# Kernel tuning notes

Hardware: AMD Instinct MI355X
Metric: run time of the kernel (lower is better)

Reference implementation:

```python
import jax, jax.numpy as jnp
import numpy as np

N_NODES = 50000
N_EDGES = 800000
N_GRAPHS = 256
IN_DIM = 128
HID = 128
BN_EPS = 1e-5


def setup_inputs() -> dict:
    key = jax.random.key(0)
    ks = jax.random.split(key, 12)
    s = 1.0 / np.sqrt(HID)
    feats = jax.random.normal(ks[0], (N_NODES, IN_DIM), jnp.float32)
    src = jax.random.randint(ks[1], (2, N_EDGES), 0, N_NODES)
    dst = jax.random.randint(ks[2], (2, N_EDGES), 0, N_NODES)
    graph_ids = jnp.sort(jax.random.randint(ks[3], (N_NODES,), 0, N_GRAPHS))
    eps = jnp.full((2, 2), 0.1, jnp.float32)
    Wa = jax.random.normal(ks[4], (2, 2, IN_DIM, HID), jnp.float32) * s
    ba = jnp.zeros((2, 2, HID), jnp.float32)
    bng = jnp.ones((2, 2, HID), jnp.float32)
    bnb = jnp.zeros((2, 2, HID), jnp.float32)
    Wb = jax.random.normal(ks[5], (2, 2, HID, HID), jnp.float32) * s
    bb = jnp.zeros((2, 2, HID), jnp.float32)
    oW1 = jax.random.normal(ks[6], (2 * HID, HID), jnp.float32) * (1.0 / np.sqrt(2 * HID))
    ob1 = jnp.zeros((HID,), jnp.float32)
    oW2 = jax.random.normal(ks[7], (HID, HID), jnp.float32) * s
    ob2 = jnp.zeros((HID,), jnp.float32)
    oW3 = jax.random.normal(ks[8], (HID, 1), jnp.float32) * s
    ob3 = jnp.zeros((1,), jnp.float32)
    return {"feats": feats, "src": src, "dst": dst, "graph_ids": graph_ids,
            "n_graphs": N_GRAPHS, "eps": eps, "Wa": Wa, "ba": ba, "bng": bng,
            "bnb": bnb, "Wb": Wb, "bb": bb, "oW1": oW1, "ob1": ob1,
            "oW2": oW2, "ob2": ob2, "oW3": oW3, "ob3": ob3}


def _gin_layer(h, s, d, eps_l, Wa_l, ba_l, g_l, be_l, Wb_l, bb_l, relu_out):
    # sum-aggregate messages from src to dst over edge list
    N = h.shape[0]
    agg = jax.ops.segment_sum(h[s], d, num_segments=N)  # [N, D]
    x = (1.0 + eps_l) * h + agg
    # MLP_Layer: Linear -> BatchNorm(training stats) -> ReLU -> Linear
    x = x @ Wa_l + ba_l
    mu = jnp.mean(x, axis=0)
    var = jnp.var(x, axis=0)
    x = (x - mu) * jax.lax.rsqrt(var + BN_EPS) * g_l + be_l
    x = jax.nn.relu(x)
    x = x @ Wb_l + bb_l
    return jax.nn.relu(x) if relu_out else x  # GINConv activation (gin1 only)


def reference(feats, src, dst, graph_ids, n_graphs, eps, Wa, ba, bng, bnb,
              Wb, bb, oW1, ob1, oW2, ob2, oW3, ob3):
    outs = []
    for e in range(2):  # one BTGINs encoder per bottom edge type
        h = feats
        for l in range(2):  # gin1 (ReLU) then gin2 (no activation)
            h = _gin_layer(h, src[e], dst[e], eps[e, l], Wa[e, l], ba[e, l],
                           bng[e, l], bnb[e, l], Wb[e, l], bb[e, l], relu_out=(l == 0))
        outs.append(h)
    h = jnp.concatenate(outs, axis=-1)  # [N, 2*HID]
    # readout_nodes op='sum': per-graph segment sum
    hg = jax.ops.segment_sum(h, graph_ids, num_segments=n_graphs)  # [G, 2*HID]
    # out_layers: 3-layer MLP, no BN
    x = jax.nn.relu(hg @ oW1 + ob1)
    x = jax.nn.relu(x @ oW2 + ob2)
    return x @ oW3 + ob3  # [G, 1]
```

## Files before the change

### kernel.cpp

```cpp
#include <hip/hip_runtime.h>

#define NT 50000
#define NE 800000
#define NG 256
#define DIM 128
#define GEMM_B ((NT + 127) / 128)

#define NB 128
#define BW 391
#define PB 196
#define PCH 4096
#define HCN (NB * PB)

typedef short s16x8 __attribute__((ext_vector_type(8)));
typedef float f32x16 __attribute__((ext_vector_type(16)));

__device__ __forceinline__ unsigned short f32_to_bf16(float f) {
    unsigned int u = __float_as_uint(f);
    u += 0x7FFFu + ((u >> 16) & 1u);
    return (unsigned short)(u >> 16);
}
__device__ __forceinline__ float bf16_to_f32(unsigned short h) {
    return __uint_as_float(((unsigned int)h) << 16);
}

__global__ __launch_bounds__(256) void ranges_kernel(const int* __restrict__ gid,
                                                     int* __restrict__ goff) {
    int g = threadIdx.x;
    int lo = 0, hi = NT;
    while (lo < hi) {
        int mid = (lo + hi) >> 1;
        if (gid[mid] < g) lo = mid + 1; else hi = mid;
    }
    goff[g] = lo;
    if (g == 0) goff[NG] = NT;
}

__global__ __launch_bounds__(256) void tobf16_kernel(const float* __restrict__ in,
                                                     unsigned short* __restrict__ out) {
    int i = blockIdx.x * 256 + threadIdx.x;
    if (i >= NT * 32) return;
    float4 v = ((const float4*)in)[i];
    ushort4 o;
    o.x = f32_to_bf16(v.x); o.y = f32_to_bf16(v.y);
    o.z = f32_to_bf16(v.z); o.w = f32_to_bf16(v.w);
    ((ushort4*)out)[i] = o;
}

__global__ __launch_bounds__(256) void csr_part_hist_kernel(
        const int* __restrict__ dstAll, int* __restrict__ hcoarseAll) {
    const int* dst = dstAll + (size_t)blockIdx.y * NE;
    int* hcoarse = hcoarseAll + (size_t)blockIdx.y * HCN;
    __shared__ int h[NB];
    if (threadIdx.x < NB) h[threadIdx.x] = 0;
    __syncthreads();
#pragma unroll
    for (int i = 0; i < PCH / 256; ++i) {
        int e = blockIdx.x * PCH + i * 256 + threadIdx.x;
        if (e < NE) atomicAdd(&h[dst[e] / BW], 1);
    }
    __syncthreads();
    if (threadIdx.x < NB)
        hcoarse[threadIdx.x * PB + blockIdx.x] = h[threadIdx.x];
}

__global__ __launch_bounds__(1024) void csr_scan_kernel(
        const int* __restrict__ hcoarseAll, int* __restrict__ offAll,
        int* __restrict__ bucketBaseAll, int* __restrict__ indptrAll) {
    const int* hcoarse = hcoarseAll + (size_t)blockIdx.x * HCN;
    int* off = offAll + (size_t)blockIdx.x * HCN;
    int* bucketBase = bucketBaseAll + (size_t)blockIdx.x * (NB + 1);
    int* indptr = indptrAll + (size_t)blockIdx.x * (NT + 1);
    __shared__ int ps[1024];
    int t = threadIdx.x;
    const int CH = (HCN + 1023) / 1024;
    int beg = t * CH, end = beg + CH; if (end > HCN) end = HCN;
    int s = 0;
    for (int i = beg; i < end; ++i) s += hcoarse[i];
    ps[t] = s;
    __syncthreads();
    for (int o = 1; o < 1024; o <<= 1) {
        int v = (t >= o) ? ps[t - o] : 0;
        __syncthreads();
        ps[t] += v;
        __syncthreads();
    }
    int run = (t == 0) ? 0 : ps[t - 1];
    for (int i = beg; i < end; ++i) {
        off[i] = run;
        if (i % PB == 0) bucketBase[i / PB] = run;
        run += hcoarse[i];
    }
    if (t == 1023) bucketBase[NB] = NE;
    if (t == 0) indptr[NT] = NE;
}

__global__ __launch_bounds__(256) void csr_scatter_kernel(
        const int* __restrict__ srcAll, const int* __restrict__ dstAll,
        const int* __restrict__ offAll, unsigned int* __restrict__ partAll) {
    const int* src = srcAll + (size_t)blockIdx.y * NE;
    const int* dst = dstAll + (size_t)blockIdx.y * NE;
    const int* off = offAll + (size_t)blockIdx.y * HCN;
    unsigned int* part = partAll + (size_t)blockIdx.y * NE;
    __shared__ int cur[NB];
    if (threadIdx.x < NB) cur[threadIdx.x] = off[threadIdx.x * PB + blockIdx.x];
    __syncthreads();
#pragma unroll
    for (int i = 0; i < PCH / 256; ++i) {
        int e = blockIdx.x * PCH + i * 256 + threadIdx.x;
        if (e < NE) {
            int d = dst[e];
            int b = d / BW;
            int pos = atomicAdd(&cur[b], 1);
            part[pos] = ((unsigned int)(d - b * BW) << 16) | (unsigned int)src[e];
        }
    }
}

__global__ __launch_bounds__(256) void csr_finalize_kernel(
        const unsigned int* __restrict__ partAll,
        const int* __restrict__ bucketBaseAll,
        int* __restrict__ indptrAll, int* __restrict__ esrcAll) {
    const unsigned int* part = partAll + (size_t)blockIdx.y * NE;
    const int* bucketBase = bucketBaseAll + (size_t)blockIdx.y * (NB + 1);
    int* indptr = indptrAll + (size_t)blockIdx.y * (NT + 1);
    int* esrc = esrcAll + (size_t)blockIdx.y * NE;
    __shared__ int cnt[512];
    __shared__ int excl[512];
    __shared__ int ps[256];
    __shared__ int cur[BW + 1];
    int b = blockIdx.x, t = threadIdx.x;
    int base = bucketBase[b];
    int n = bucketBase[b + 1] - base;
    cnt[t] = 0; cnt[t + 256] = 0;
    for (int j = t; j <= BW; j += 256) cur[j] = 0;
    __syncthreads();
    for (int i = t; i < n; i += 256) atomicAdd(&cnt[part[base + i] >> 16], 1);
    __syncthreads();
    int a0 = cnt[2 * t], a1 = cnt[2 * t + 1];
    ps[t] = a0 + a1;
    __syncthreads();
    for (int o = 1; o < 256; o <<= 1) {
        int v = (t >= o) ? ps[t - o] : 0;
        __syncthreads();
        ps[t] += v;
        __syncthreads();
    }
    int before = (t == 0) ? 0 : ps[t - 1];
    excl[2 * t] = before;
    excl[2 * t + 1] = before + a0;
    __syncthreads();
    int node0 = b * BW;
    for (int j = t; j < BW; j += 256) {
        int gn = node0 + j;
        if (gn < NT) indptr[gn] = base + excl[j];
    }
    for (int i = t; i < n; i += 256) {
        unsigned int pk = part[base + i];
        int dl = pk >> 16;
        int pos = atomicAdd(&cur[dl], 1);
        esrc[base + excl[dl] + pos] = (int)(pk & 0xFFFFu);
    }
}

__global__ __launch_bounds__(256) void agg_split_kernel(
        const float* __restrict__ h,
        const unsigned short* __restrict__ hb,
        const int* __restrict__ indptr, const int* __restrict__ esrc,
        const float* __restrict__ eps_p, int eps_idx,
        unsigned short* __restrict__ xout) {
    int node = blockIdx.x * 8 + (threadIdx.x >> 5);
    int lane = threadIdx.x & 31;
    if (node >= NT) return;
    float e1 = 1.0f + eps_p[eps_idx];
    float4 a = ((const float4*)h)[(size_t)node * 32 + lane];
    float s0 = e1 * a.x, s1 = e1 * a.y, s2 = e1 * a.z, s3 = e1 * a.w;
    int beg = indptr[node], end = indptr[node + 1];
    int j = beg;
    for (; j + 8 <= end; j += 8) {
        ushort4 v0 = *(const ushort4*)(hb + (size_t)esrc[j + 0] * 128 + lane * 4);
        ushort4 v1 = *(const ushort4*)(hb + (size_t)esrc[j + 1] * 128 + lane * 4);
        ushort4 v2 = *(const ushort4*)(hb + (size_t)esrc[j + 2] * 128 + lane * 4);
        ushort4 v3 = *(const ushort4*)(hb + (size_t)esrc[j + 3] * 128 + lane * 4);
        ushort4 v4 = *(const ushort4*)(hb + (size_t)esrc[j + 4] * 128 + lane * 4);
        ushort4 v5 = *(const ushort4*)(hb + (size_t)esrc[j + 5] * 128 + lane * 4);
        ushort4 v6 = *(const ushort4*)(hb + (size_t)esrc[j + 6] * 128 + lane * 4);
        ushort4 v7 = *(const ushort4*)(hb + (size_t)esrc[j + 7] * 128 + lane * 4);
        s0 += ((bf16_to_f32(v0.x) + bf16_to_f32(v1.x)) + (bf16_to_f32(v2.x) + bf16_to_f32(v3.x)))
            + ((bf16_to_f32(v4.x) + bf16_to_f32(v5.x)) + (bf16_to_f32(v6.x) + bf16_to_f32(v7.x)));
        s1 += ((bf16_to_f32(v0.y) + bf16_to_f32(v1.y)) + (bf16_to_f32(v2.y) + bf16_to_f32(v3.y)))
            + ((bf16_to_f32(v4.y) + bf16_to_f32(v5.y)) + (bf16_to_f32(v6.y) + bf16_to_f32(v7.y)));
        s2 += ((bf16_to_f32(v0.z) + bf16_to_f32(v1.z)) + (bf16_to_f32(v2.z) + bf16_to_f32(v3.z)))
            + ((bf16_to_f32(v4.z) + bf16_to_f32(v5.z)) + (bf16_to_f32(v6.z) + bf16_to_f32(v7.z)));
        s3 += ((bf16_to_f32(v0.w) + bf16_to_f32(v1.w)) + (bf16_to_f32(v2.w) + bf16_to_f32(v3.w)))
            + ((bf16_to_f32(v4.w) + bf16_to_f32(v5.w)) + (bf16_to_f32(v6.w) + bf16_to_f32(v7.w)));
    }
    for (; j + 2 <= end; j += 2) {
        ushort4 v0 = *(const ushort4*)(hb + (size_t)esrc[j + 0] * 128 + lane * 4);
        ushort4 v1 = *(const ushort4*)(hb + (size_t)esrc[j + 1] * 128 + lane * 4);
        s0 += bf16_to_f32(v0.x) + bf16_to_f32(v1.x);
        s1 += bf16_to_f32(v0.y) + bf16_to_f32(v1.y);
        s2 += bf16_to_f32(v0.z) + bf16_to_f32(v1.z);
        s3 += bf16_to_f32(v0.w) + bf16_to_f32(v1.w);
    }
    if (j < end) {
        ushort4 v0 = *(const ushort4*)(hb + (size_t)esrc[j] * 128 + lane * 4);
        s0 += bf16_to_f32(v0.x); s1 += bf16_to_f32(v0.y);
        s2 += bf16_to_f32(v0.z); s3 += bf16_to_f32(v0.w);
    }
    ushort4 hv, lv;
    hv.x = f32_to_bf16(s0); lv.x = f32_to_bf16(s0 - bf16_to_f32(hv.x));
    hv.y = f32_to_bf16(s1); lv.y = f32_to_bf16(s1 - bf16_to_f32(hv.y));
    hv.z = f32_to_bf16(s2); lv.z = f32_to_bf16(s2 - bf16_to_f32(hv.z));
    hv.w = f32_to_bf16(s3); lv.w = f32_to_bf16(s3 - bf16_to_f32(hv.w));
    *(ushort4*)(xout + (size_t)node * 256 + lane * 4) = hv;
    *(ushort4*)(xout + (size_t)node * 256 + 128 + lane * 4) = lv;
}

__global__ __launch_bounds__(256) void bsplit_kernel(const float* __restrict__ Wa,
                                                     const float* __restrict__ Wb,
                                                     unsigned short* __restrict__ Bfrag) {
    int slot = blockIdx.x >> 3;
    int sub = blockIdx.x & 7;
    const float* W = (slot < 4) ? (Wa + (size_t)slot * DIM * DIM)
                                : (Wb + (size_t)(slot - 4) * DIM * DIM);
    unsigned short* out = Bfrag + (size_t)slot * 32768;
    for (int i = 0; i < 16; ++i) {
        int e = sub * 4096 + i * 256 + threadIdx.x;
        int kphys = e >> 7, n = e & 127;
        int k = kphys & 127;
        float wv = W[k * 128 + n];
        unsigned short hi = f32_to_bf16(wv);
        unsigned short val = (kphys < 128) ? hi : f32_to_bf16(wv - bf16_to_f32(hi));
        int nt = n >> 5, nin = n & 31;
        int kcp = kphys >> 4, kgp = (kphys >> 3) & 1, jj = kphys & 7;
        out[(size_t)(((nt * 16 + kcp) * 64) + kgp * 32 + nin) * 8 + jj] = val;
    }
}

template <int ASPLIT, int STATS, int RELU, int EMITB>
__global__ __launch_bounds__(256) void fused_gemm_kernel(
        const void* __restrict__ Asrc,
        const unsigned short* __restrict__ Bfrag,
        const float* __restrict__ bias,
        const float* __restrict__ gsumIn, const float* __restrict__ gamma,
        const float* __restrict__ beta,
        float* __restrict__ C, unsigned short* __restrict__ CBout,
        float* __restrict__ gsum, float* __restrict__ gsumsq) {
    __shared__ char smem[65536 + 1024];
    unsigned short* sB = (unsigned short*)smem;
    float* sBNa = (float*)(smem + 65536);
    float* sBNb = sBNa + 128;
    const int tid = threadIdx.x;
    const int w = tid >> 6, lane = tid & 63;
    const int nin = lane & 31, kg = lane >> 5;
    const int row0 = blockIdx.x * 128;
    const int myrow = row0 + w * 32 + nin;
    const int rowc = myrow < NT ? myrow : NT - 1;

    {
        const uint4* Bg = (const uint4*)Bfrag;
        uint4* sB4 = (uint4*)smem;
#pragma unroll
        for (int i = 0; i < 16; ++i) sB4[tid + 256 * i] = Bg[tid + 256 * i];
    }

    s16x8 ahi[8], alo[8];
    if (ASPLIT) {
        const unsigned short* ar = (const unsigned short*)Asrc + (size_t)rowc * 256 + kg * 8;
#pragma unroll
        for (int kc = 0; kc < 8; ++kc) {
            ahi[kc] = *(const s16x8*)(ar + kc * 16);
            alo[kc] = *(const s16x8*)(ar + 128 + kc * 16);
        }
        __syncthreads();
    } else {
        if (tid < 128) {
            float mu = gsumIn[tid] * (1.0f / NT);
            float var = gsumIn[128 + tid] * (1.0f / NT) - mu * mu;
            float inv = rsqrtf(var + 1e-5f);
            float a = gamma[tid] * inv;
            sBNa[tid] = a;
            sBNb[tid] = beta[tid] - mu * a;
        }
        __syncthreads();
        const float* yr = (const float*)Asrc + (size_t)rowc * 128 + kg * 8;
#pragma unroll
        for (int kc = 0; kc < 8; ++kc) {
            int c0 = kc * 16 + kg * 8;
            float4 y0 = *(const float4*)(yr + kc * 16);
            float4 y1 = *(const float4*)(yr + kc * 16 + 4);
            float4 a0 = *(const float4*)(sBNa + c0);
            float4 a1 = *(const float4*)(sBNa + c0 + 4);
            float4 b0 = *(const float4*)(sBNb + c0);
            float4 b1 = *(const float4*)(sBNb + c0 + 4);
            float t[8];
            t[0] = fmaxf(0.f, fmaf(y0.x, a0.x, b0.x));
            t[1] = fmaxf(0.f, fmaf(y0.y, a0.y, b0.y));
            t[2] = fmaxf(0.f, fmaf(y0.z, a0.z, b0.z));
            t[3] = fmaxf(0.f, fmaf(y0.w, a0.w, b0.w));
            t[4] = fmaxf(0.f, fmaf(y1.x, a1.x, b1.x));
            t[5] = fmaxf(0.f, fmaf(y1.y, a1.y, b1.y));
            t[6] = fmaxf(0.f, fmaf(y1.z, a1.z, b1.z));
            t[7] = fmaxf(0.f, fmaf(y1.w, a1.w, b1.w));
            union { s16x8 v; unsigned short u[8]; } H, L;
#pragma unroll
            for (int q = 0; q < 8; ++q) {
                H.u[q] = f32_to_bf16(t[q]);
                L.u[q] = f32_to_bf16(t[q] - bf16_to_f32(H.u[q]));
            }
            ahi[kc] = H.v; alo[kc] = L.v;
        }
    }

    f32x16 acc[4];
#pragma unroll
    for (int nt = 0; nt < 4; ++nt)
#pragma unroll
        for (int r = 0; r < 16; ++r) acc[nt][r] = 0.f;

#pragma unroll
    for (int nt = 0; nt < 4; ++nt) {
        const unsigned short* bp = sB + (size_t)(nt * 16) * 512 + lane * 8;
#pragma unroll
        for (int kc = 0; kc < 8; ++kc) {
            s16x8 b = *(const s16x8*)(bp + kc * 512);
            acc[nt] = __builtin_amdgcn_mfma_f32_32x32x16_bf16(ahi[kc], b, acc[nt], 0, 0, 0);
            acc[nt] = __builtin_amdgcn_mfma_f32_32x32x16_bf16(alo[kc], b, acc[nt], 0, 0, 0);
        }
#pragma unroll
        for (int kc = 0; kc < 8; ++kc) {
            s16x8 b = *(const s16x8*)(bp + (8 + kc) * 512);
            acc[nt] = __builtin_amdgcn_mfma_f32_32x32x16_bf16(ahi[kc], b, acc[nt], 0, 0, 0);
        }
    }

    const int rbase = row0 + w * 32 + 4 * kg;
#pragma unroll
    for (int nt = 0; nt < 4; ++nt) {
        int col = nt * 32 + nin;
        float bv = bias[col];
#pragma unroll
        for (int reg = 0; reg < 16; ++reg) {
            int gr = rbase + (reg & 3) + 8 * (reg >> 2);
            float v = acc[nt][reg] + bv;
            if (RELU) v = fmaxf(v, 0.f);
            if (gr < NT) {
                C[(size_t)gr * 128 + col] = v;
                if (EMITB) CBout[(size_t)gr * 128 + col] = f32_to_bf16(v);
            }
            acc[nt][reg] = (gr < NT) ? v : 0.f;
        }
    }

    if (STATS) {
        __syncthreads();
        float* ls = (float*)smem;
        ls[tid] = 0.f;
        __syncthreads();
#pragma unroll
        for (int nt = 0; nt < 4; ++nt) {
            int col = nt * 32 + nin;
            float s = 0.f, q = 0.f;
#pragma unroll
            for (int reg = 0; reg < 16; ++reg) { float v = acc[nt][reg]; s += v; q += v * v; }
            atomicAdd(&ls[col], s);
            atomicAdd(&ls[128 + col], q);
        }
        __syncthreads();
        if (tid < 128) {
            atomicAdd(&gsum[tid], ls[tid]);
            atomicAdd(&gsumsq[tid], ls[128 + tid]);
        }
    }
}

__global__ __launch_bounds__(256) void readout_kernel(const float* __restrict__ h,
                                                      const int* __restrict__ goff,
                                                      float* __restrict__ hgp,
                                                      int colOff) {
    int g = blockIdx.x >> 1, h2 = blockIdx.x & 1;
    int c = threadIdx.x & 127, rr = threadIdx.x >> 7;
    int beg = goff[g], end = goff[g + 1];
    int n = beg + h2 * 2 + rr;
    float a0 = 0.f, a1 = 0.f, a2 = 0.f, a3 = 0.f;
    for (; n + 12 < end; n += 16) {
        a0 += h[(size_t)n * 128 + c];
        a1 += h[(size_t)(n + 4) * 128 + c];
        a2 += h[(size_t)(n + 8) * 128 + c];
        a3 += h[(size_t)(n + 12) * 128 + c];
    }
    for (; n < end; n += 4) a0 += h[(size_t)n * 128 + c];
    float acc = (a0 + a1) + (a2 + a3);
    __shared__ float ls[256];
    ls[threadIdx.x] = acc;
    __syncthreads();
    if (threadIdx.x < 128)
        hgp[(size_t)h2 * NG * 256 + g * 256 + colOff + c] = ls[c] + ls[128 + c];
}

__global__ __launch_bounds__(128) void mlp_kernel(const float* __restrict__ hgp,
                                                  const float* __restrict__ oW1,
                                                  const float* __restrict__ ob1,
                                                  const float* __restrict__ oW2,
                                                  const float* __restrict__ ob2,
                                                  const float* __restrict__ oW3,
                                                  const float* __restrict__ ob3,
                                                  float* __restrict__ out) {
    int g = blockIdx.x, t = threadIdx.x;
    __shared__ float sh[256];
    __shared__ float z[128];
    sh[t] = hgp[g * 256 + t] + hgp[(size_t)NG * 256 + g * 256 + t];
    sh[t + 128] = hgp[g * 256 + 128 + t] + hgp[(size_t)NG * 256 + g * 256 + 128 + t];
    __syncthreads();
    float acc = ob1[t];
    for (int k = 0; k < 256; ++k) acc = fmaf(sh[k], oW1[k * 128 + t], acc);
    float z1 = fmaxf(acc, 0.f);
    z[t] = z1;
    __syncthreads();
    acc = ob2[t];
    for (int k = 0; k < 128; ++k) acc = fmaf(z[k], oW2[k * 128 + t], acc);
    float z2 = fmaxf(acc, 0.f);
    float p = z2 * oW3[t];
    for (int off = 32; off > 0; off >>= 1) p += __shfl_down(p, off, 64);
    __shared__ float wsum[2];
    if ((t & 63) == 0) wsum[t >> 6] = p;
    __syncthreads();
    if (t == 0) out[g] = wsum[0] + wsum[1] + ob3[0];
}

extern "C" void kernel_launch(void* const* d_in, const int* in_sizes, int n_in,
                              void* d_out, int out_size, void* d_ws, size_t ws_size,
                              hipStream_t stream) {
    (void)in_sizes; (void)n_in; (void)out_size; (void)ws_size;
    const float* feats = (const float*)d_in[0];
    const int*   src   = (const int*)d_in[1];
    const int*   dst   = (const int*)d_in[2];
    const int*   gid   = (const int*)d_in[3];
    const float* epsp  = (const float*)d_in[5];
    const float* Wa    = (const float*)d_in[6];
    const float* ba    = (const float*)d_in[7];
    const float* bng   = (const float*)d_in[8];
    const float* bnb   = (const float*)d_in[9];
    const float* Wb    = (const float*)d_in[10];
    const float* bb    = (const float*)d_in[11];
    const float* oW1   = (const float*)d_in[12];
    const float* ob1   = (const float*)d_in[13];
    const float* oW2   = (const float*)d_in[14];
    const float* ob2   = (const float*)d_in[15];
    const float* oW3   = (const float*)d_in[16];
    const float* ob3   = (const float*)d_in[17];
    float* out = (float*)d_out;

    char* p = (char*)d_ws;
    auto carve = [&](size_t bytes) -> void* {
        void* r = (void*)p;
        p += (bytes + 255) & ~(size_t)255;
        return r;
    };
    unsigned short* Asplit = (unsigned short*)carve((size_t)NT * 256 * 2);
    float* bufY    = (float*)carve((size_t)NT * DIM * 4);
    float* bufH    = (float*)carve((size_t)NT * DIM * 4);
    unsigned short* featsB = (unsigned short*)carve((size_t)NT * DIM * 2);
    unsigned short* hB     = (unsigned short*)carve((size_t)NT * DIM * 2);
    unsigned short* Bfrag  = (unsigned short*)carve((size_t)8 * 32768 * 2);
    int*   esrc2    = (int*)carve((size_t)2 * NE * 4);
    unsigned int* part2 = (unsigned int*)carve((size_t)2 * NE * 4);
    int*   hcoarse2 = (int*)carve((size_t)2 * HCN * 4);
    int*   offbuf2  = (int*)carve((size_t)2 * HCN * 4);
    int*   bb2      = (int*)carve((size_t)2 * (NB + 1) * 4);
    int*   indptr2  = (int*)carve((size_t)2 * (NT + 1) * 4);
    int*   goff     = (int*)carve((size_t)(NG + 1) * 4);
    float* gsumAll  = (float*)carve((size_t)4 * 256 * 4);
    float* hgp      = (float*)carve((size_t)2 * NG * 256 * 4);

    const int CB = (NT * 32 + 255) / 256;

    ranges_kernel<<<1, 256, 0, stream>>>(gid, goff);
    bsplit_kernel<<<64, 256, 0, stream>>>(Wa, Wb, Bfrag);
    tobf16_kernel<<<CB, 256, 0, stream>>>(feats, featsB);
    hipMemsetAsync(gsumAll, 0, (size_t)4 * 256 * 4, stream);

    csr_part_hist_kernel<<<dim3(PB, 2), 256, 0, stream>>>(dst, hcoarse2);
    csr_scan_kernel<<<2, 1024, 0, stream>>>(hcoarse2, offbuf2, bb2, indptr2);
    csr_scatter_kernel<<<dim3(PB, 2), 256, 0, stream>>>(src, dst, offbuf2, part2);
    csr_finalize_kernel<<<dim3(NB, 2), 256, 0, stream>>>(part2, bb2, indptr2, esrc2);

    for (int e = 0; e < 2; ++e) {
        const int* indptr = indptr2 + (size_t)e * (NT + 1);
        const int* esrc   = esrc2 + (size_t)e * NE;
        for (int l = 0; l < 2; ++l) {
            int wi = e * 2 + l;
            float* gsum = gsumAll + wi * 256;
            float* gsumsq = gsum + 128;
            const float* hSrc = (l == 0) ? feats : bufH;
            const unsigned short* hbSrc = (l == 0) ? featsB : hB;
            agg_split_kernel<<<(NT + 7) / 8, 256, 0, stream>>>(
                hSrc, hbSrc, indptr, esrc, epsp, wi, Asplit);
            fused_gemm_kernel<1, 1, 0, 0><<<GEMM_B, 256, 0, stream>>>(
                Asplit, Bfrag + (size_t)wi * 32768, ba + (size_t)wi * DIM,
                nullptr, nullptr, nullptr, bufY, nullptr, gsum, gsumsq);
            if (l == 0)
                fused_gemm_kernel<0, 0, 1, 1><<<GEMM_B, 256, 0, stream>>>(
                    bufY, Bfrag + (size_t)(4 + wi) * 32768, bb + (size_t)wi * DIM,
                    gsum, bng + (size_t)wi * DIM, bnb + (size_t)wi * DIM,
                    bufH, hB, nullptr, nullptr);
            else
                fused_gemm_kernel<0, 0, 0, 0><<<GEMM_B, 256, 0, stream>>>(
                    bufY, Bfrag + (size_t)(4 + wi) * 32768, bb + (size_t)wi * DIM,
                    gsum, bng + (size_t)wi * DIM, bnb + (size_t)wi * DIM,
                    bufH, nullptr, nullptr, nullptr);
        }
        readout_kernel<<<NG * 2, 256, 0, stream>>>(bufH, goff, hgp, e * 128);
    }
    mlp_kernel<<<NG, 128, 0, stream>>>(hgp, oW1, ob1, oW2, ob2, oW3, ob3, out);
}
```

Before: 550.7 us.

## Batch both edge-type encoders into single launches and split edges across half-waves

Runs the two encoder branches together by adding a blockIdx.y dimension to the aggregation, GEMM and readout kernels, which halves the number of launches and doubles the grid per launch. The per-branch buffers are duplicated so both branches can live in memory at once. The aggregation kernel now gives each node a full 64-lane wave: the two 32-lane halves take alternating edges and combine their sums with a cross-half shuffle, which should expose more memory-level parallelism in the gather. The cost is a larger workspace, and half the lanes sit idle during the final bf16 split and store.

```diff
diff --git a/kernel.cpp b/kernel.cpp
--- a/kernel.cpp
+++ b/kernel.cpp
@@ -164,28 +164,38 @@
 }
 
 __global__ __launch_bounds__(256) void agg_split_kernel(
-        const float* __restrict__ h,
-        const unsigned short* __restrict__ hb,
-        const int* __restrict__ indptr, const int* __restrict__ esrc,
-        const float* __restrict__ eps_p, int eps_idx,
-        unsigned short* __restrict__ xout) {
-    int node = blockIdx.x * 8 + (threadIdx.x >> 5);
-    int lane = threadIdx.x & 31;
+        const float* __restrict__ h, long hStride,
+        const unsigned short* __restrict__ hb, long hbStride,
+        const int* __restrict__ indptr2, const int* __restrict__ esrc2,
+        const float* __restrict__ eps_p, int l,
+        unsigned short* __restrict__ xout2) {
+    int e = blockIdx.y;
+    const float* hs = h + (size_t)e * hStride;
+    const unsigned short* hbs = hb + (size_t)e * hbStride;
+    const int* indptr = indptr2 + (size_t)e * (NT + 1);
+    const int* esrc = esrc2 + (size_t)e * NE;
+    unsigned short* xo = xout2 + (size_t)e * NT * 256;
+    int node = blockIdx.x * 4 + (threadIdx.x >> 6);
     if (node >= NT) return;
-    float e1 = 1.0f + eps_p[eps_idx];
-    float4 a = ((const float4*)h)[(size_t)node * 32 + lane];
-    float s0 = e1 * a.x, s1 = e1 * a.y, s2 = e1 * a.z, s3 = e1 * a.w;
+    int lane = threadIdx.x & 63;
+    int half = lane >> 5, c = lane & 31;
+    float s0 = 0.f, s1 = 0.f, s2 = 0.f, s3 = 0.f;
+    if (half == 0) {
+        float e1 = 1.0f + eps_p[e * 2 + l];
+        float4 a = ((const float4*)hs)[(size_t)node * 32 + c];
+        s0 = e1 * a.x; s1 = e1 * a.y; s2 = e1 * a.z; s3 = e1 * a.w;
+    }
     int beg = indptr[node], end = indptr[node + 1];
-    int j = beg;
-    for (; j + 8 <= end; j += 8) {
-        ushort4 v0 = *(const ushort4*)(hb + (size_t)esrc[j + 0] * 128 + lane * 4);
-        ushort4 v1 = *(const ushort4*)(hb + (size_t)esrc[j + 1] * 128 + lane * 4);
-        ushort4 v2 = *(const ushort4*)(hb + (size_t)esrc[j + 2] * 128 + lane * 4);
-        ushort4 v3 = *(const ushort4*)(hb + (size_t)esrc[j + 3] * 128 + lane * 4);
-        ushort4 v4 = *(const ushort4*)(hb + (size_t)esrc[j + 4] * 128 + lane * 4);
-        ushort4 v5 = *(const ushort4*)(hb + (size_t)esrc[j + 5] * 128 + lane * 4);
-        ushort4 v6 = *(const ushort4*)(hb + (size_t)esrc[j + 6] * 128 + lane * 4);
-        ushort4 v7 = *(const ushort4*)(hb + (size_t)esrc[j + 7] * 128 + lane * 4);
+    int j = beg + half;
+    for (; j + 14 < end; j += 16) {
+        ushort4 v0 = *(const ushort4*)(hbs + (size_t)esrc[j + 0] * 128 + c * 4);
+        ushort4 v1 = *(const ushort4*)(hbs + (size_t)esrc[j + 2] * 128 + c * 4);
+        ushort4 v2 = *(const ushort4*)(hbs + (size_t)esrc[j + 4] * 128 + c * 4);
+        ushort4 v3 = *(const ushort4*)(hbs + (size_t)esrc[j + 6] * 128 + c * 4);
+        ushort4 v4 = *(const ushort4*)(hbs + (size_t)esrc[j + 8] * 128 + c * 4);
+        ushort4 v5 = *(const ushort4*)(hbs + (size_t)esrc[j + 10] * 128 + c * 4);
+        ushort4 v6 = *(const ushort4*)(hbs + (size_t)esrc[j + 12] * 128 + c * 4);
+        ushort4 v7 = *(const ushort4*)(hbs + (size_t)esrc[j + 14] * 128 + c * 4);
         s0 += ((bf16_to_f32(v0.x) + bf16_to_f32(v1.x)) + (bf16_to_f32(v2.x) + bf16_to_f32(v3.x)))
             + ((bf16_to_f32(v4.x) + bf16_to_f32(v5.x)) + (bf16_to_f32(v6.x) + bf16_to_f32(v7.x)));
         s1 += ((bf16_to_f32(v0.y) + bf16_to_f32(v1.y)) + (bf16_to_f32(v2.y) + bf16_to_f32(v3.y)))
@@ -195,26 +205,24 @@
         s3 += ((bf16_to_f32(v0.w) + bf16_to_f32(v1.w)) + (bf16_to_f32(v2.w) + bf16_to_f32(v3.w)))
             + ((bf16_to_f32(v4.w) + bf16_to_f32(v5.w)) + (bf16_to_f32(v6.w) + bf16_to_f32(v7.w)));
     }
-    for (; j + 2 <= end; j += 2) {
-        ushort4 v0 = *(const ushort4*)(hb + (size_t)esrc[j + 0] * 128 + lane * 4);
-        ushort4 v1 = *(const ushort4*)(hb + (size_t)esrc[j + 1] * 128 + lane * 4);
-        s0 += bf16_to_f32(v0.x) + bf16_to_f32(v1.x);
-        s1 += bf16_to_f32(v0.y) + bf16_to_f32(v1.y);
-        s2 += bf16_to_f32(v0.z) + bf16_to_f32(v1.z);
-        s3 += bf16_to_f32(v0.w) + bf16_to_f32(v1.w);
-    }
-    if (j < end) {
-        ushort4 v0 = *(const ushort4*)(hb + (size_t)esrc[j] * 128 + lane * 4);
+    for (; j < end; j += 2) {
+        ushort4 v0 = *(const ushort4*)(hbs + (size_t)esrc[j] * 128 + c * 4);
         s0 += bf16_to_f32(v0.x); s1 += bf16_to_f32(v0.y);
         s2 += bf16_to_f32(v0.z); s3 += bf16_to_f32(v0.w);
     }
-    ushort4 hv, lv;
-    hv.x = f32_to_bf16(s0); lv.x = f32_to_bf16(s0 - bf16_to_f32(hv.x));
-    hv.y = f32_to_bf16(s1); lv.y = f32_to_bf16(s1 - bf16_to_f32(hv.y));
-    hv.z = f32_to_bf16(s2); lv.z = f32_to_bf16(s2 - bf16_to_f32(hv.z));
-    hv.w = f32_to_bf16(s3); lv.w = f32_to_bf16(s3 - bf16_to_f32(hv.w));
-    *(ushort4*)(xout + (size_t)node * 256 + lane * 4) = hv;
-    *(ushort4*)(xout + (size_t)node * 256 + 128 + lane * 4) = lv;
+    s0 += __shfl_xor(s0, 32);
+    s1 += __shfl_xor(s1, 32);
+    s2 += __shfl_xor(s2, 32);
+    s3 += __shfl_xor(s3, 32);
+    if (half == 0) {
+        ushort4 hv, lv;
+        hv.x = f32_to_bf16(s0); lv.x = f32_to_bf16(s0 - bf16_to_f32(hv.x));
+        hv.y = f32_to_bf16(s1); lv.y = f32_to_bf16(s1 - bf16_to_f32(hv.y));
+        hv.z = f32_to_bf16(s2); lv.z = f32_to_bf16(s2 - bf16_to_f32(hv.z));
+        hv.w = f32_to_bf16(s3); lv.w = f32_to_bf16(s3 - bf16_to_f32(hv.w));
+        *(ushort4*)(xo + (size_t)node * 256 + c * 4) = hv;
+        *(ushort4*)(xo + (size_t)node * 256 + 128 + c * 4) = lv;
+    }
 }
 
 __global__ __launch_bounds__(256) void bsplit_kernel(const float* __restrict__ Wa,
@@ -240,17 +248,21 @@
 
 template <int ASPLIT, int STATS, int RELU, int EMITB>
 __global__ __launch_bounds__(256) void fused_gemm_kernel(
-        const void* __restrict__ Asrc,
-        const unsigned short* __restrict__ Bfrag,
-        const float* __restrict__ bias,
-        const float* __restrict__ gsumIn, const float* __restrict__ gamma,
-        const float* __restrict__ beta,
-        float* __restrict__ C, unsigned short* __restrict__ CBout,
-        float* __restrict__ gsum, float* __restrict__ gsumsq) {
+        const void* __restrict__ Asrc, long aStride,
+        const unsigned short* __restrict__ BfragBase, int bOff, int l,
+        const float* __restrict__ biasBase,
+        const float* __restrict__ gsumBase,
+        const float* __restrict__ gammaBase, const float* __restrict__ betaBase,
+        float* __restrict__ C, long cStride,
+        unsigned short* __restrict__ CBout, long cbStride,
+        float* __restrict__ gsumOutBase) {
     __shared__ char smem[65536 + 1024];
     unsigned short* sB = (unsigned short*)smem;
     float* sBNa = (float*)(smem + 65536);
     float* sBNb = sBNa + 128;
+    const int ety = blockIdx.y, wi = ety * 2 + l;
+    const unsigned short* Bfrag = BfragBase + (size_t)(bOff + wi) * 32768;
+    const float* bias = biasBase + (size_t)wi * DIM;
     const int tid = threadIdx.x;
     const int w = tid >> 6, lane = tid & 63;
     const int nin = lane & 31, kg = lane >> 5;
@@ -267,7 +279,8 @@
 
     s16x8 ahi[8], alo[8];
     if (ASPLIT) {
-        const unsigned short* ar = (const unsigned short*)Asrc + (size_t)rowc * 256 + kg * 8;
+        const unsigned short* ar = (const unsigned short*)Asrc
+                + (size_t)ety * aStride + (size_t)rowc * 256 + kg * 8;
 #pragma unroll
         for (int kc = 0; kc < 8; ++kc) {
             ahi[kc] = *(const s16x8*)(ar + kc * 16);
@@ -275,16 +288,18 @@
         }
         __syncthreads();
     } else {
+        const float* gsumIn = gsumBase + (size_t)wi * 256;
         if (tid < 128) {
             float mu = gsumIn[tid] * (1.0f / NT);
             float var = gsumIn[128 + tid] * (1.0f / NT) - mu * mu;
             float inv = rsqrtf(var + 1e-5f);
-            float a = gamma[tid] * inv;
+            float a = gammaBase[wi * DIM + tid] * inv;
             sBNa[tid] = a;
-            sBNb[tid] = beta[tid] - mu * a;
-        }
-        __syncthreads();
-        const float* yr = (const float*)Asrc + (size_t)rowc * 128 + kg * 8;
+            sBNb[tid] = betaBase[wi * DIM + tid] - mu * a;
+        }
+        __syncthreads();
+        const float* yr = (const float*)Asrc + (size_t)ety * aStride
+                + (size_t)rowc * 128 + kg * 8;
 #pragma unroll
         for (int kc = 0; kc < 8; ++kc) {
             int c0 = kc * 16 + kg * 8;
@@ -335,6 +350,8 @@
         }
     }
 
+    float* Ce = C + (size_t)ety * cStride;
+    unsigned short* CBe = EMITB ? (CBout + (size_t)ety * cbStride) : nullptr;
     const int rbase = row0 + w * 32 + 4 * kg;
 #pragma unroll
     for (int nt = 0; nt < 4; ++nt) {
@@ -346,14 +363,15 @@
             float v = acc[nt][reg] + bv;
             if (RELU) v = fmaxf(v, 0.f);
             if (gr < NT) {
-                C[(size_t)gr * 128 + col] = v;
-                if (EMITB) CBout[(size_t)gr * 128 + col] = f32_to_bf16(v);
+                Ce[(size_t)gr * 128 + col] = v;
+                if (EMITB) CBe[(size_t)gr * 128 + col] = f32_to_bf16(v);
             }
             acc[nt][reg] = (gr < NT) ? v : 0.f;
         }
     }
 
     if (STATS) {
+        float* gsum = gsumOutBase + (size_t)wi * 256;
         __syncthreads();
         float* ls = (float*)smem;
         ls[tid] = 0.f;
@@ -370,15 +388,17 @@
         __syncthreads();
         if (tid < 128) {
             atomicAdd(&gsum[tid], ls[tid]);
-            atomicAdd(&gsumsq[tid], ls[128 + tid]);
-        }
-    }
-}
-
-__global__ __launch_bounds__(256) void readout_kernel(const float* __restrict__ h,
+            atomicAdd(&gsum[128 + tid], ls[128 + tid]);
+        }
+    }
+}
+
+__global__ __launch_bounds__(256) void readout_kernel(const float* __restrict__ bufH2,
                                                       const int* __restrict__ goff,
-                                                      float* __restrict__ hgp,
-                                                      int colOff) {
+                                                      float* __restrict__ hgp) {
+    int e = blockIdx.y;
+    const float* h = bufH2 + (size_t)e * NT * 128;
+    int colOff = e * 128;
     int g = blockIdx.x >> 1, h2 = blockIdx.x & 1;
     int c = threadIdx.x & 127, rr = threadIdx.x >> 7;
     int beg = goff[g], end = goff[g + 1];
@@ -458,11 +478,11 @@
         p += (bytes + 255) & ~(size_t)255;
         return r;
     };
-    unsigned short* Asplit = (unsigned short*)carve((size_t)NT * 256 * 2);
-    float* bufY    = (float*)carve((size_t)NT * DIM * 4);
-    float* bufH    = (float*)carve((size_t)NT * DIM * 4);
+    unsigned short* Asplit2 = (unsigned short*)carve((size_t)2 * NT * 256 * 2);
+    float* bufY2   = (float*)carve((size_t)2 * NT * DIM * 4);
+    float* bufH2   = (float*)carve((size_t)2 * NT * DIM * 4);
     unsigned short* featsB = (unsigned short*)carve((size_t)NT * DIM * 2);
-    unsigned short* hB     = (unsigned short*)carve((size_t)NT * DIM * 2);
+    unsigned short* hB2    = (unsigned short*)carve((size_t)2 * NT * DIM * 2);
     unsigned short* Bfrag  = (unsigned short*)carve((size_t)8 * 32768 * 2);
     int*   esrc2    = (int*)carve((size_t)2 * NE * 4);
     unsigned int* part2 = (unsigned int*)carve((size_t)2 * NE * 4);
@@ -486,32 +506,29 @@
     csr_scatter_kernel<<<dim3(PB, 2), 256, 0, stream>>>(src, dst, offbuf2, part2);
     csr_finalize_kernel<<<dim3(NB, 2), 256, 0, stream>>>(part2, bb2, indptr2, esrc2);
 
-    for (int e = 0; e < 2; ++e) {
-        const int* indptr = indptr2 + (size_t)e * (NT + 1);
-        const int* esrc   = esrc2 + (size_t)e * NE;
-        for (int l = 0; l < 2; ++l) {
-            int wi = e * 2 + l;
-            float* gsum = gsumAll + wi * 256;
-            float* gsumsq = gsum + 128;
-            const float* hSrc = (l == 0) ? feats : bufH;
-            const unsigned short* hbSrc = (l == 0) ? featsB : hB;
-            agg_split_kernel<<<(NT + 7) / 8, 256, 0, stream>>>(
-                hSrc, hbSrc, indptr, esrc, epsp, wi, Asplit);
-            fused_gemm_kernel<1, 1, 0, 0><<<GEMM_B, 256, 0, stream>>>(
-                Asplit, Bfrag + (size_t)wi * 32768, ba + (size_t)wi * DIM,
-                nullptr, nullptr, nullptr, bufY, nullptr, gsum, gsumsq);
-            if (l == 0)
-                fused_gemm_kernel<0, 0, 1, 1><<<GEMM_B, 256, 0, stream>>>(
-                    bufY, Bfrag + (size_t)(4 + wi) * 32768, bb + (size_t)wi * DIM,
-                    gsum, bng + (size_t)wi * DIM, bnb + (size_t)wi * DIM,
-                    bufH, hB, nullptr, nullptr);
-            else
-                fused_gemm_kernel<0, 0, 0, 0><<<GEMM_B, 256, 0, stream>>>(
-                    bufY, Bfrag + (size_t)(4 + wi) * 32768, bb + (size_t)wi * DIM,
-                    gsum, bng + (size_t)wi * DIM, bnb + (size_t)wi * DIM,
-                    bufH, nullptr, nullptr, nullptr);
-        }
-        readout_kernel<<<NG * 2, 256, 0, stream>>>(bufH, goff, hgp, e * 128);
-    }
+    for (int l = 0; l < 2; ++l) {
+        if (l == 0)
+            agg_split_kernel<<<dim3((NT + 3) / 4, 2), 256, 0, stream>>>(
+                feats, 0, featsB, 0, indptr2, esrc2, epsp, l, Asplit2);
+        else
+            agg_split_kernel<<<dim3((NT + 3) / 4, 2), 256, 0, stream>>>(
+                bufH2, (long)NT * DIM, hB2, (long)NT * DIM,
+                indptr2, esrc2, epsp, l, Asplit2);
+        fused_gemm_kernel<1, 1, 0, 0><<<dim3(GEMM_B, 2), 256, 0, stream>>>(
+            Asplit2, (long)NT * 256, Bfrag, 0, l, ba,
+            nullptr, nullptr, nullptr,
+            bufY2, (long)NT * DIM, nullptr, 0, gsumAll);
+        if (l == 0)
+            fused_gemm_kernel<0, 0, 1, 1><<<dim3(GEMM_B, 2), 256, 0, stream>>>(
+                bufY2, (long)NT * DIM, Bfrag, 4, l, bb,
+                gsumAll, bng, bnb,
+                bufH2, (long)NT * DIM, hB2, (long)NT * DIM, nullptr);
+        else
+            fused_gemm_kernel<0, 0, 0, 0><<<dim3(GEMM_B, 2), 256, 0, stream>>>(
+                bufY2, (long)NT * DIM, Bfrag, 4, l, bb,
+                gsumAll, bng, bnb,
+                bufH2, (long)NT * DIM, nullptr, 0, nullptr);
+    }
+    readout_kernel<<<dim3(NG * 2, 2), 256, 0, stream>>>(bufH2, goff, hgp);
     mlp_kernel<<<NG, 128, 0, stream>>>(hgp, oW1, ob1, oW2, ob2, oW3, ob3, out);
 }
```

Result: no change. 554.2 us (+0.6%).
